# Performance work log

Hardware: AMD Instinct MI355X
Metric: run time of the kernel (lower is better)

The kernel has to match this reference:

```python
import jax, jax.numpy as jnp
import numpy as np

D = 1024
N = 4096
K = 16


def setup_inputs() -> dict:
    key = jax.random.key(0)
    ks = jax.random.split(key, 10)
    s = 1.0 / np.sqrt(3 * D)
    return {
        "token": jax.random.normal(ks[0], (N, D), jnp.float32),
        "routed_tokens": jax.random.normal(ks[1], (N, K, D), jnp.float32),
        "sim_row": jax.random.normal(ks[2], (N, K), jnp.float32),
        "delta_emb": jax.random.normal(ks[3], (N, K, D), jnp.float32),
        "W_logic": jax.random.uniform(ks[4], (3 * D, D), jnp.float32, -s, s),
        "b_logic": jax.random.uniform(ks[5], (D,), jnp.float32, -s, s),
        "ln_gamma": jnp.ones((D,), jnp.float32),
        "ln_beta": jnp.zeros((D,), jnp.float32),
        "W_gate": jax.random.uniform(ks[6], (3 * D, D), jnp.float32, -s, s),
        "b_gate": jax.random.uniform(ks[7], (D,), jnp.float32, -s, s),
    }


def _layernorm(x, gamma, beta, eps=1e-5):
    mu = jnp.mean(x, axis=-1, keepdims=True)
    var = jnp.mean(jnp.square(x - mu), axis=-1, keepdims=True)
    return (x - mu) * jax.lax.rsqrt(var + eps) * gamma + beta


def reference(token, routed_tokens, sim_row, delta_emb,
              W_logic, b_logic, ln_gamma, ln_beta, W_gate, b_gate):
    n, k, d = routed_tokens.shape
    token_exp = jnp.broadcast_to(token[:, None, :], (n, k, d))
    combined = jnp.concatenate([token_exp, routed_tokens, delta_emb], axis=-1)  # [N,K,3D]
    h = jnp.einsum('nke,ed->nkd', combined, W_logic) + b_logic
    fused = _layernorm(jax.nn.gelu(h, approximate=False), ln_gamma, ln_beta)  # [N,K,D]
    sim_w = jax.nn.softmax(sim_row, axis=-1)  # [N,K]
    arg_summary = jnp.einsum('nk,nkd->nd', sim_w, fused)  # [N,D]
    gate_in = jnp.concatenate([token, arg_summary, arg_summary], axis=-1)  # [N,3D]
    gate = jax.nn.sigmoid(gate_in @ W_gate + b_gate)  # [N,D]
    return (arg_summary, gate)
```

## Files before the change

### kernel.cpp

```cpp
#include <hip/hip_runtime.h>
#include <hip/hip_bf16.h>


typedef __attribute__((ext_vector_type(4))) float f32x4;
typedef __attribute__((ext_vector_type(2))) float f32x2;
typedef __attribute__((ext_vector_type(8))) short bf16x8;

__device__ __forceinline__ ushort f2bf(float f) {
  unsigned b = __builtin_bit_cast(unsigned, f);
  b += 0x7FFFu + ((b >> 16) & 1u);
  return (ushort)(b >> 16);
}
__device__ __forceinline__ unsigned pk2(float a, float b) {
  return (unsigned)f2bf(a) | ((unsigned)f2bf(b) << 16);
}

__device__ __forceinline__ unsigned swz(unsigned a) {
  return a ^ (((a >> 7) & 3u) << 4);
}

__device__ __forceinline__ f32x2 ntld2(const float* p) {
  return __builtin_nontemporal_load((const f32x2*)p);
}

__global__ __launch_bounds__(256) void prep_kernel(
    const float* __restrict__ Wl, const float* __restrict__ Wg,
    const float* __restrict__ token,
    ushort* __restrict__ Bmain, ushort* __restrict__ Bk1,
    ushort* __restrict__ Bgate, ushort* __restrict__ tokenb) {
  int t = threadIdx.x;
  int bid = blockIdx.x;
  if (bid >= 1280) {
    size_t base = (size_t)(bid - 1280) * 16384;
#pragma unroll
    for (int it = 0; it < 16; ++it) {
      size_t e = base + (size_t)it * 1024 + t * 4;
      f32x4 v = *(const f32x4*)(token + e);
      uint2 o; o.x = pk2(v[0], v[1]); o.y = pk2(v[2], v[3]);
      *(uint2*)(tokenb + e) = o;
    }
    return;
  }
  __shared__ float L[32][129];
  const float* src; int row0, mode, kt, wg; ushort* dst;
  if (bid < 512)      { mode = 0; kt = bid >> 3;        wg = bid & 7; src = Wl; row0 = 1024 + kt * 32; dst = Bmain; }
  else if (bid < 768) { mode = 1; kt = (bid - 512) >> 3; wg = (bid - 512) & 7; src = Wl; row0 = kt * 32; dst = Bk1; }
  else                { mode = 2; kt = (bid - 768) >> 3; wg = (bid - 768) & 7; src = Wg; row0 = kt * 32; dst = Bgate; }
  int col0 = wg * 128;
  bool dosum = (mode == 2) && (kt >= 32);
#pragma unroll
  for (int p = 0; p < 4; ++p) {
    int r = p * 8 + (t >> 5), c = (t & 31) * 4;
    const float* sp = src + (size_t)(row0 + r) * 1024 + col0 + c;
    f32x4 v = *(const f32x4*)sp;
    if (dosum) { f32x4 v2 = *(const f32x4*)(sp + (size_t)1024 * 1024); v += v2; }
    L[r][c] = v[0]; L[r][c + 1] = v[1]; L[r][c + 2] = v[2]; L[r][c + 3] = v[3];
  }
  __syncthreads();
  if (mode == 0) {
    for (int c = t; c < 512; c += 256) {
      int nf = c >> 6, lane = c & 63, lr_ = lane & 15, lh_ = lane >> 4;
      bf16x8 o;
#pragma unroll
      for (int m = 0; m < 8; ++m) o[m] = (short)f2bf(L[lh_ * 8 + m][nf * 16 + lr_]);
      *(bf16x8*)(dst + (size_t)kt * 32768 + wg * 4096 + c * 8) = o;
    }
  } else {
    for (int c = t; c < 512; c += 256) {
      int nn = c >> 2, q = c & 3;
      bf16x8 o;
#pragma unroll
      for (int m = 0; m < 8; ++m) o[m] = (short)f2bf(L[q * 8 + m][nn]);
      *(bf16x8*)(dst + (size_t)kt * 32768 + (size_t)(wg * 128 + nn) * 32 + q * 8) = o;
    }
  }
}

template <int NKT, int NSPLIT, int ACT>
__global__ __launch_bounds__(256) void gemm_small_b(
    const ushort* __restrict__ A0, const ushort* __restrict__ A1,
    const ushort* __restrict__ Bp, const float* __restrict__ bias,
    float* __restrict__ Cout) {
  int tid = threadIdx.x, l = tid & 63, wid = tid >> 6;
  int wm = wid & 1, wn = wid >> 1;
  int mbase = blockIdx.x * 64 + wm * 32;
  int nbase = blockIdx.y * 128 + wn * 64;
  int lr = l & 15, lh = l >> 4;
  f32x4 acc[2][4] = {};
#pragma unroll 1
  for (int kt = 0; kt < NKT; ++kt) {
    const ushort* As = (kt < NSPLIT) ? A0 : A1;
    int ke = ((kt < NSPLIT) ? kt : kt - NSPLIT) * 32 + lh * 8;
    bf16x8 af[2];
#pragma unroll
    for (int mf = 0; mf < 2; ++mf)
      af[mf] = *(const bf16x8*)(As + (size_t)(mbase + mf * 16 + lr) * 1024 + ke);
    bf16x8 bf[4];
#pragma unroll
    for (int nf = 0; nf < 4; ++nf)
      bf[nf] = *(const bf16x8*)(Bp + (size_t)kt * 32768 +
                                (size_t)(nbase + nf * 16 + lr) * 32 + lh * 8);
#pragma unroll
    for (int nf = 0; nf < 4; ++nf)
#pragma unroll
      for (int mf = 0; mf < 2; ++mf)
        acc[mf][nf] = __builtin_amdgcn_mfma_f32_16x16x32_bf16(
            af[mf], bf[nf], acc[mf][nf], 0, 0, 0);
  }
#pragma unroll
  for (int nf = 0; nf < 4; ++nf) {
    int col = nbase + nf * 16 + lr;
    float bs = bias[col];
#pragma unroll
    for (int mf = 0; mf < 2; ++mf)
#pragma unroll
      for (int j = 0; j < 4; ++j) {
        int row = mbase + mf * 16 + lh * 4 + j;
        float v = acc[mf][nf][j] + bs;
        if (ACT == 1) v = 1.0f / (1.0f + expf(-v));
        Cout[(size_t)row * 1024 + col] = v;
      }
  }
}

#define MFMA_STEP(ABSYM, BF) do {                                         \
  const char* ab_ = (const char*)(ABSYM) + aoff0;                         \
  bf16x8 af_[4];                                                          \
  _Pragma("unroll")                                                       \
  for (int mf = 0; mf < 4; ++mf)                                          \
    af_[mf] = *(const bf16x8*)(ab_ + mf * 1024);                          \
  _Pragma("unroll")                                                       \
  for (int nf = 0; nf < 4; ++nf)                                          \
    _Pragma("unroll")                                                     \
    for (int mf = 0; mf < 4; ++mf)                                        \
      acc[mf][nf] = __builtin_amdgcn_mfma_f32_16x16x32_bf16(              \
          af_[mf], (BF)[nf], acc[mf][nf], 0, 0, 0);                       \
} while (0)

#define BARRIER_LG() do {                                                 \
  asm volatile("s_waitcnt lgkmcnt(0)" ::: "memory");                      \
  __builtin_amdgcn_s_barrier();                                           \
  asm volatile("" ::: "memory");                                          \
} while (0)

__global__ __launch_bounds__(1024) void main_kernel(
    const float* __restrict__ routed, const float* __restrict__ delta,
    const float* __restrict__ simrow, const ushort* __restrict__ Bmain,
    const float* __restrict__ tpart, const float* __restrict__ gamma,
    const float* __restrict__ beta, float* __restrict__ out_arg,
    ushort* __restrict__ argb) {
  __shared__ ushort Ab0[2048];
  __shared__ ushort Ab1[2048];
  __shared__ float ldsW[64];
  __shared__ float lnS[64 * 16], lnQ[64 * 16];

  int tid = threadIdx.x, l = tid & 63, wid = tid >> 6;
  int bx = blockIdx.x;
  int lr = l & 15, lh = l >> 4;

  if (tid < 4) {
    int n = bx * 4 + tid;
    float sv[16], mx = -1e30f;
#pragma unroll
    for (int j = 0; j < 16; ++j) { sv[j] = simrow[n * 16 + j]; mx = fmaxf(mx, sv[j]); }
    float s = 0.f;
#pragma unroll
    for (int j = 0; j < 16; ++j) { sv[j] = expf(sv[j] - mx); s += sv[j]; }
    float inv = 1.0f / s;
#pragma unroll
    for (int j = 0; j < 16; ++j) ldsW[tid * 16 + j] = sv[j] * inv;
  }

  const float* rbase = routed + (size_t)(bx * 64 + (tid >> 4)) * 1024 + (tid & 15) * 2;
  const float* dbase = delta  + (size_t)(bx * 64 + (tid >> 4)) * 1024 + (tid & 15) * 2;
  const unsigned adst = swz((unsigned)tid * 4);

  const unsigned aoff0 = swz((unsigned)lr * 64 + (unsigned)lh * 16);

  const ushort* bptr = Bmain + (size_t)(wid >> 1) * 4096 +
                       (size_t)(wid & 1) * 2048 + (size_t)l * 8;

  f32x2 t0 = ntld2(rbase);
  f32x2 avA = ntld2(rbase + 32);
  f32x2 avB;
  bf16x8 bfA[4], bfB[4];
#pragma unroll
  for (int nf = 0; nf < 4; ++nf)
    bfA[nf] = *(const bf16x8*)(bptr + nf * 512);
  *(unsigned*)((char*)Ab0 + adst) = pk2(t0[0], t0[1]);
  BARRIER_LG();

  f32x4 acc[4][4] = {};
#pragma unroll 1
  for (int kt = 0; kt < 64; kt += 2) {
    {
      const float* as_ = (kt + 2 < 32) ? rbase : dbase;
      avB = ntld2(as_ + (size_t)((kt + 2) & 31) * 32);
    }
#pragma unroll
    for (int nf = 0; nf < 4; ++nf)
      bfB[nf] = *(const bf16x8*)(bptr + 32768 + nf * 512);
    *(unsigned*)((char*)Ab1 + adst) = pk2(avA[0], avA[1]);
    MFMA_STEP(Ab0, bfA);
    BARRIER_LG();
    {
      const float* as_ = (kt + 3 < 32) ? rbase : dbase;
      avA = ntld2(as_ + (size_t)((kt + 3) & 31) * 32);
    }
#pragma unroll
    for (int nf = 0; nf < 4; ++nf)
      bfA[nf] = *(const bf16x8*)(bptr + 65536 + nf * 512);
    *(unsigned*)((char*)Ab0 + adst) = pk2(avB[0], avB[1]);
    MFMA_STEP(Ab1, bfB);
    BARRIER_LG();
    bptr += 65536;
  }

  const float inv_d = 1.0f / 1024.0f;
  float gam[4], bet[4];
#pragma unroll
  for (int nf = 0; nf < 4; ++nf) {
    int c = wid * 64 + nf * 16 + lr;
    gam[nf] = gamma[c]; bet[nf] = beta[c];
  }
#pragma unroll
  for (int mf = 0; mf < 4; ++mf) {
    int tokrow = bx * 4 + mf;
    float s[4] = {0, 0, 0, 0}, q[4] = {0, 0, 0, 0};
#pragma unroll
    for (int nf = 0; nf < 4; ++nf) {
      float tp = __builtin_nontemporal_load(
          tpart + (size_t)tokrow * 1024 + wid * 64 + nf * 16 + lr);
#pragma unroll
      for (int j = 0; j < 4; ++j) {
        float h = acc[mf][nf][j] + tp;
        float u = h * (1.5957691f + 0.07135481f * h * h);
        float g = h / (1.0f + __expf(-u));
        acc[mf][nf][j] = g;
        s[j] += g; q[j] += g * g;
      }
    }
#pragma unroll
    for (int j = 0; j < 4; ++j) {
#pragma unroll
      for (int d = 1; d <= 8; d <<= 1) {
        s[j] += __shfl_xor(s[j], d, 64);
        q[j] += __shfl_xor(q[j], d, 64);
      }
    }
    if (lr == 0) {
#pragma unroll
      for (int j = 0; j < 4; ++j) {
        int row = mf * 16 + lh * 4 + j;
        lnS[row * 16 + wid] = s[j];
        lnQ[row * 16 + wid] = q[j];
      }
    }
  }
  __syncthreads();
#pragma unroll
  for (int mf = 0; mf < 4; ++mf) {
    float mu[4], rs[4], wk[4];
#pragma unroll
    for (int j = 0; j < 4; ++j) {
      int row = mf * 16 + lh * 4 + j;
      float S = 0.f, Q = 0.f;
#pragma unroll
      for (int w4 = 0; w4 < 4; ++w4) {
        f32x4 vs = *(const f32x4*)&lnS[row * 16 + w4 * 4];
        f32x4 vq = *(const f32x4*)&lnQ[row * 16 + w4 * 4];
        S += vs[0] + vs[1] + vs[2] + vs[3];
        Q += vq[0] + vq[1] + vq[2] + vq[3];
      }
      float m_ = S * inv_d;
      mu[j] = m_;
      rs[j] = rsqrtf(Q * inv_d - m_ * m_ + 1e-5f);
      wk[j] = ldsW[row];
    }
#pragma unroll
    for (int nf = 0; nf < 4; ++nf) {
      float ws = 0.f;
#pragma unroll
      for (int j = 0; j < 4; ++j) {
        float y = (acc[mf][nf][j] - mu[j]) * rs[j] * gam[nf] + bet[nf];
        ws += wk[j] * y;
      }
      ws += __shfl_xor(ws, 16, 64);
      ws += __shfl_xor(ws, 32, 64);
      if (lh == 0) {
        size_t oidx = (size_t)(bx * 4 + mf) * 1024 + wid * 64 + nf * 16 + lr;
        out_arg[oidx] = ws;
        argb[oidx] = f2bf(ws);
      }
    }
  }
}

extern "C" void kernel_launch(void* const* d_in, const int* in_sizes, int n_in,
                              void* d_out, int out_size, void* d_ws, size_t ws_size,
                              hipStream_t stream) {
  const float* token  = (const float*)d_in[0];
  const float* routed = (const float*)d_in[1];
  const float* simrow = (const float*)d_in[2];
  const float* delta  = (const float*)d_in[3];
  const float* Wl     = (const float*)d_in[4];
  const float* bl     = (const float*)d_in[5];
  const float* gamma  = (const float*)d_in[6];
  const float* beta   = (const float*)d_in[7];
  const float* Wg     = (const float*)d_in[8];
  const float* bg     = (const float*)d_in[9];

  char* ws = (char*)d_ws;
  ushort* Bmain  = (ushort*)(ws);
  ushort* Bk1    = (ushort*)(ws + (4u << 20));
  ushort* Bgate  = (ushort*)(ws + (6u << 20));
  float*  tpart  = (float*)(ws + (10u << 20));
  ushort* tokenb = (ushort*)(ws + (26u << 20));
  ushort* argb   = (ushort*)(ws + (34u << 20));

  float* out_arg  = (float*)d_out;
  float* out_gate = out_arg + (size_t)4096 * 1024;

  prep_kernel<<<1536, 256, 0, stream>>>(Wl, Wg, token, Bmain, Bk1, Bgate, tokenb);
  gemm_small_b<32, 32, 0><<<dim3(64, 8), 256, 0, stream>>>(
      tokenb, tokenb, Bk1, bl, tpart);
  main_kernel<<<1024, 1024, 0, stream>>>(
      routed, delta, simrow, Bmain, tpart, gamma, beta, out_arg, argb);
  gemm_small_b<64, 32, 1><<<dim3(64, 8), 256, 0, stream>>>(
      tokenb, argb, Bgate, bg, out_gate);
}
```

Before: 479.4 us.

## Stage full 64x1024 A half-tiles in LDS instead of per-k double buffering

Replaces the per-k-step double-buffered A tile (with a barrier every step) with bulk staging. Each half of the A operand (routed, then delta), 64 rows by 1024 bf16, goes into 128KB of dynamic LDS using 16-byte swizzled writes. The MFMA loop then runs over that half with no barriers, and only four __syncthreads remain in total. This removes the per-iteration barrier and small 8-byte global loads, at the cost of exposed load latency during staging and a large LDS footprint that limits the kernel to one block per CU.

```diff
diff --git a/kernel.cpp b/kernel.cpp
--- a/kernel.cpp
+++ b/kernel.cpp
@@ -13,14 +13,6 @@
 }
 __device__ __forceinline__ unsigned pk2(float a, float b) {
   return (unsigned)f2bf(a) | ((unsigned)f2bf(b) << 16);
-}
-
-__device__ __forceinline__ unsigned swz(unsigned a) {
-  return a ^ (((a >> 7) & 3u) << 4);
-}
-
-__device__ __forceinline__ f32x2 ntld2(const float* p) {
-  return __builtin_nontemporal_load((const f32x2*)p);
 }
 
 __global__ __launch_bounds__(256) void prep_kernel(
@@ -123,24 +115,65 @@
   }
 }
 
-#define MFMA_STEP(ABSYM, BF) do {                                         \
-  const char* ab_ = (const char*)(ABSYM) + aoff0;                         \
-  bf16x8 af_[4];                                                          \
-  _Pragma("unroll")                                                       \
-  for (int mf = 0; mf < 4; ++mf)                                          \
-    af_[mf] = *(const bf16x8*)(ab_ + mf * 1024);                          \
-  _Pragma("unroll")                                                       \
-  for (int nf = 0; nf < 4; ++nf)                                          \
-    _Pragma("unroll")                                                     \
-    for (int mf = 0; mf < 4; ++mf)                                        \
-      acc[mf][nf] = __builtin_amdgcn_mfma_f32_16x16x32_bf16(              \
-          af_[mf], (BF)[nf], acc[mf][nf], 0, 0, 0);                       \
+#define STAGE_HALF(SRC) do {                                               \
+  const float* sr_ = (SRC) + (size_t)(bx * 64 + arow) * 1024 + acol * 8;   \
+  char* lw_ = smem + arow * 2048;                                          \
+  unsigned xw_ = (unsigned)(arow & 7) << 4;                                \
+  _Pragma("unroll 4")                                                      \
+  for (int j = 0; j < 8; ++j) {                                            \
+    f32x4 va_ = __builtin_nontemporal_load((const f32x4*)(sr_ + j * 128)); \
+    f32x4 vb_ = __builtin_nontemporal_load((const f32x4*)(sr_ + j * 128 + 4)); \
+    uint4 o_;                                                              \
+    o_.x = pk2(va_[0], va_[1]); o_.y = pk2(va_[2], va_[3]);                \
+    o_.z = pk2(vb_[0], vb_[1]); o_.w = pk2(vb_[2], vb_[3]);                \
+    unsigned kb_ = ((unsigned)(acol * 16 + j * 256)) ^ xw_;                \
+    *(uint4*)(lw_ + kb_) = o_;                                             \
+  }                                                                        \
 } while (0)
 
-#define BARRIER_LG() do {                                                 \
-  asm volatile("s_waitcnt lgkmcnt(0)" ::: "memory");                      \
-  __builtin_amdgcn_s_barrier();                                           \
-  asm volatile("" ::: "memory");                                          \
+#define HALF_LOOP(KT0) do {                                                \
+  const ushort* bp_ = Bmain + (size_t)(KT0) * 32768 + boff;                \
+  bf16x8 bfA_[4], bfB_[4];                                                 \
+  _Pragma("unroll")                                                        \
+  for (int nf = 0; nf < 4; ++nf)                                           \
+    bfA_[nf] = *(const bf16x8*)(bp_ + nf * 512);                           \
+  _Pragma("unroll 1")                                                      \
+  for (int kt = 0; kt < 32; kt += 2) {                                     \
+    _Pragma("unroll")                                                      \
+    for (int nf = 0; nf < 4; ++nf)                                         \
+      bfB_[nf] = *(const bf16x8*)(bp_ + (size_t)(kt + 1) * 32768 + nf * 512); \
+    {                                                                      \
+      unsigned ko_ = ((unsigned)(kt << 6) + lh16) ^ xr;                    \
+      const char* ab_ = abase + ko_;                                       \
+      bf16x8 af_[4];                                                       \
+      _Pragma("unroll")                                                    \
+      for (int mf = 0; mf < 4; ++mf)                                       \
+        af_[mf] = *(const bf16x8*)(ab_ + mf * 32768);                      \
+      _Pragma("unroll")                                                    \
+      for (int nf = 0; nf < 4; ++nf)                                       \
+        _Pragma("unroll")                                                  \
+        for (int mf = 0; mf < 4; ++mf)                                     \
+          acc[mf][nf] = __builtin_amdgcn_mfma_f32_16x16x32_bf16(           \
+              af_[mf], bfA_[nf], acc[mf][nf], 0, 0, 0);                    \
+    }                                                                      \
+    _Pragma("unroll")                                                      \
+    for (int nf = 0; nf < 4; ++nf)    \
+      bfA_[nf] = *(const bf16x8*)(bp_ + (size_t)(kt + 2) * 32768 + nf * 512); \
+    {                                                                      \
+      unsigned ko_ = ((unsigned)((kt + 1) << 6) + lh16) ^ xr;              \
+      const char* ab_ = abase + ko_;                                       \
+      bf16x8 af_[4];                                                       \
+      _Pragma("unroll")                                                    \
+      for (int mf = 0; mf < 4; ++mf)                                       \
+        af_[mf] = *(const bf16x8*)(ab_ + mf * 32768);                      \
+      _Pragma("unroll")                                                    \
+      for (int nf = 0; nf < 4; ++nf)                                       \
+        _Pragma("unroll")                                                  \
+        for (int mf = 0; mf < 4; ++mf)                                     \
+          acc[mf][nf] = __builtin_amdgcn_mfma_f32_16x16x32_bf16(           \
+              af_[mf], bfB_[nf], acc[mf][nf], 0, 0, 0);                    \
+    }                                                                      \
+  }                                                                        \
 } while (0)
 
 __global__ __launch_bounds__(1024) void main_kernel(
@@ -149,10 +182,10 @@
     const float* __restrict__ tpart, const float* __restrict__ gamma,
     const float* __restrict__ beta, float* __restrict__ out_arg,
     ushort* __restrict__ argb) {
-  __shared__ ushort Ab0[2048];
-  __shared__ ushort Ab1[2048];
-  __shared__ float ldsW[64];
-  __shared__ float lnS[64 * 16], lnQ[64 * 16];
+  extern __shared__ char smem[];
+  float* ldsW = (float*)(smem + 131072);
+  float* lnS = (float*)smem;
+  float* lnQ = (float*)(smem + 4096);
 
   int tid = threadIdx.x, l = tid & 63, wid = tid >> 6;
   int bx = blockIdx.x;
@@ -171,50 +204,26 @@
     for (int j = 0; j < 16; ++j) ldsW[tid * 16 + j] = sv[j] * inv;
   }
 
-  const float* rbase = routed + (size_t)(bx * 64 + (tid >> 4)) * 1024 + (tid & 15) * 2;
-  const float* dbase = delta  + (size_t)(bx * 64 + (tid >> 4)) * 1024 + (tid & 15) * 2;
-  const unsigned adst = swz((unsigned)tid * 4);
-
-  const unsigned aoff0 = swz((unsigned)lr * 64 + (unsigned)lh * 16);
-
-  const ushort* bptr = Bmain + (size_t)(wid >> 1) * 4096 +
-                       (size_t)(wid & 1) * 2048 + (size_t)l * 8;
-
-  f32x2 t0 = ntld2(rbase);
-  f32x2 avA = ntld2(rbase + 32);
-  f32x2 avB;
-  bf16x8 bfA[4], bfB[4];
-#pragma unroll
-  for (int nf = 0; nf < 4; ++nf)
-    bfA[nf] = *(const bf16x8*)(bptr + nf * 512);
-  *(unsigned*)((char*)Ab0 + adst) = pk2(t0[0], t0[1]);
-  BARRIER_LG();
+  const int arow = tid >> 4;
+  const int acol = tid & 15;
+
+  const unsigned xr = (unsigned)(lr & 7) << 4;
+  const unsigned lh16 = (unsigned)lh * 16;
+  const char* abase = smem + lr * 2048;
+
+  const size_t boff = (size_t)(wid >> 1) * 4096 + (size_t)(wid & 1) * 2048 +
+                      (size_t)l * 8;
 
   f32x4 acc[4][4] = {};
-#pragma unroll 1
-  for (int kt = 0; kt < 64; kt += 2) {
-    {
-      const float* as_ = (kt + 2 < 32) ? rbase : dbase;
-      avB = ntld2(as_ + (size_t)((kt + 2) & 31) * 32);
-    }
-#pragma unroll
-    for (int nf = 0; nf < 4; ++nf)
-      bfB[nf] = *(const bf16x8*)(bptr + 32768 + nf * 512);
-    *(unsigned*)((char*)Ab1 + adst) = pk2(avA[0], avA[1]);
-    MFMA_STEP(Ab0, bfA);
-    BARRIER_LG();
-    {
-      const float* as_ = (kt + 3 < 32) ? rbase : dbase;
-      avA = ntld2(as_ + (size_t)((kt + 3) & 31) * 32);
-    }
-#pragma unroll
-    for (int nf = 0; nf < 4; ++nf)
-      bfA[nf] = *(const bf16x8*)(bptr + 65536 + nf * 512);
-    *(unsigned*)((char*)Ab0 + adst) = pk2(avB[0], avB[1]);
-    MFMA_STEP(Ab1, bfB);
-    BARRIER_LG();
-    bptr += 65536;
-  }
+
+  STAGE_HALF(routed);
+  __syncthreads();
+  HALF_LOOP(0);
+  __syncthreads();
+  STAGE_HALF(delta);
+  __syncthreads();
+  HALF_LOOP(32);
+  __syncthreads();
 
   const float inv_d = 1.0f / 1024.0f;
   float gam[4], bet[4];
@@ -321,10 +330,14 @@
   float* out_arg  = (float*)d_out;
   float* out_gate = out_arg + (size_t)4096 * 1024;
 
+  const int SMEM = 131328;
+  hipFuncSetAttribute(reinterpret_cast<const void*>(main_kernel),
+                      hipFuncAttributeMaxDynamicSharedMemorySize, SMEM);
+
   prep_kernel<<<1536, 256, 0, stream>>>(Wl, Wg, token, Bmain, Bk1, Bgate, tokenb);
   gemm_small_b<32, 32, 0><<<dim3(64, 8), 256, 0, stream>>>(
       tokenb, tokenb, Bk1, bl, tpart);
-  main_kernel<<<1024, 1024, 0, stream>>>(
+  main_kernel<<<1024, 1024, SMEM, stream>>>(
       routed, delta, simrow, Bmain, tpart, gamma, beta, out_arg, argb);
   gemm_small_b<64, 32, 1><<<dim3(64, 8), 256, 0, stream>>>(
       tokenb, argb, Bgate, bg, out_gate);
```

Result: no change. 476.3 us (-0.6%).
